# Kernel tuning notes

Measured on AMD Instinct MI355X. Metric: run time of the kernel, lower is better.

Reference implementation:

```python
import jax, jax.numpy as jnp
import numpy as np

N = 8192      # nodes
D = 256       # feature dim
E = 131072    # edges (avg degree 16)
T = 1.0       # integration horizon (single RK4 step, torchdiffeq default grid)
GAMMA = -1.0  # self-loop edge weight override


def setup_inputs() -> dict:
    key = jax.random.key(0)
    k1, k2, k3, k4 = jax.random.split(key, 4)
    h = jax.random.normal(k1, (N, D), dtype=jnp.float32)
    e = jax.random.uniform(k2, (E, 1), dtype=jnp.float32)
    src = jax.random.randint(k3, (E,), 0, N, dtype=jnp.int32)
    dst = jax.random.randint(k4, (E,), 0, N, dtype=jnp.int32)
    return {"h": h, "e": e, "src": src, "dst": dst}


def reference(h, e, src, dst):
    n = h.shape[0]
    # e[src == dst] = gamma  (self-loop override)
    e = jnp.where((src == dst)[:, None], jnp.asarray(GAMMA, e.dtype), e)

    def spmm(x):
        # DGL update_all(u_mul_e('x','e','m'), sum('m','x')):
        # out[v] = sum_{(u,v) in E} e_uv * x[u]
        return jax.ops.segment_sum(e * x[src], dst, num_segments=n)

    # ODE state is (x [N,D], K [N,N]); dx/dt = spmm(x), dK/dt = x @ x.T.
    # torchdiffeq 'rk4' = 3/8-rule fixed step; t grid [0, T] -> one step of size T.
    dt = jnp.asarray(T, h.dtype)
    x0 = h
    k1x = spmm(x0)
    xb = x0 + dt * (k1x / 3.0)
    k2x = spmm(xb)
    xc = x0 + dt * (k2x - k1x / 3.0)
    k3x = spmm(xc)
    xd = x0 + dt * (k1x - k2x + k3x)
    # K0 = 0, so final K = dt/8 * (K1 + 3*(K2 + K3) + K4), Ki = xi @ xi.T
    gram = lambda x: x @ x.T
    K = dt * 0.125 * (gram(x0) + 3.0 * (gram(xb) + gram(xc)) + gram(xd))
    return K  # [N, N], the k[:, -N:] slice returned by ODEBlock
```

## Files before the change

kernel.cpp:

```cpp
#include <hip/hip_runtime.h>
#include <hip/hip_bf16.h>
#include <stdint.h>

#define NN 8192
#define DD 256
#define EE 131072
#define KK 1024
#define BKT 32
#define NT 32
#define CAP 128

typedef __attribute__((ext_vector_type(8))) short short8;
typedef __attribute__((ext_vector_type(4))) float f32x4;

#define S1 0.35355339059327373f
#define S3 0.6123724356957945f

__device__ inline short f2bf(float x) {
  __hip_bfloat16 b = __float2bfloat16(x);
  union { __hip_bfloat16 b; short s; } u; u.b = b; return u.s;
}
__device__ inline float bf2f(short x) {
  union { unsigned u; float f; } c; c.u = ((unsigned)(unsigned short)x) << 16; return c.f;
}
__device__ inline void async_load16(const void* g, void* l) {
  __builtin_amdgcn_global_load_lds((const __attribute__((address_space(1))) void*)g,
                                   (__attribute__((address_space(3))) void*)l, 16, 0, 0);
}

__global__ void clear_k(int* __restrict__ cursor) {
  cursor[blockIdx.x * 256 + threadIdx.x] = 0;
}

__global__ void scatter_edges(const int* __restrict__ src, const int* __restrict__ dst,
                              const float* __restrict__ e, int* __restrict__ cursor,
                              int2* __restrict__ edges) {
  int i = blockIdx.x * 256 + threadIdx.x;
  if (i >= EE) return;
  int d = dst[i], s = src[i];
  int pos = atomicAdd(&cursor[d], 1);
  if (pos < CAP) {
    float w = (s == d) ? -1.0f : e[i];
    union { float f; int i; } wb; wb.f = w;
    edges[d * CAP + pos] = make_int2(s, wb.i);
  }
}

__global__ void spmm1_k(const float* __restrict__ h, const int* __restrict__ cursor,
                        const int2* __restrict__ edges, float* __restrict__ k1,
                        short* __restrict__ xbb, short* __restrict__ Y) {
  int tid = blockIdx.x * 256 + threadIdx.x;
  int v = tid >> 6, lane = tid & 63;
  int cnt = min(cursor[v], CAP);
  const int2* ev = &edges[v * CAP];
  float ax = 0.f, ay = 0.f, az = 0.f, aw = 0.f;
  for (int j = 0; j < cnt; ++j) {
    int2 ed = ev[j];
    union { int i; float f; } wb; wb.i = ed.y; float w = wb.f;
    float4 xv = *reinterpret_cast<const float4*>(&h[ed.x * DD + lane * 4]);
    ax += w * xv.x; ay += w * xv.y; az += w * xv.z; aw += w * xv.w;
  }
  int idx = v * DD + lane * 4;
  float4 hv = *reinterpret_cast<const float4*>(&h[idx]);
  float4 k; k.x = ax; k.y = ay; k.z = az; k.w = aw;
  *reinterpret_cast<float4*>(&k1[idx]) = k;
  float bx = hv.x + ax * (1.f / 3.f), by = hv.y + ay * (1.f / 3.f);
  float bz = hv.z + az * (1.f / 3.f), bw = hv.w + aw * (1.f / 3.f);
  short4 xb4; xb4.x = f2bf(bx); xb4.y = f2bf(by); xb4.z = f2bf(bz); xb4.w = f2bf(bw);
  *reinterpret_cast<short4*>(&xbb[idx]) = xb4;
  short4 y0; y0.x = f2bf(S1 * hv.x); y0.y = f2bf(S1 * hv.y);
  y0.z = f2bf(S1 * hv.z); y0.w = f2bf(S1 * hv.w);
  *reinterpret_cast<short4*>(&Y[(size_t)v * KK + lane * 4]) = y0;
  short4 yb; yb.x = f2bf(S3 * bx); yb.y = f2bf(S3 * by);
  yb.z = f2bf(S3 * bz); yb.w = f2bf(S3 * bw);
  *reinterpret_cast<short4*>(&Y[(size_t)v * KK + DD + lane * 4]) = yb;
}

__global__ void spmm2_k(const short* __restrict__ xbb, const float* __restrict__ h,
                        const float* __restrict__ k1, const int* __restrict__ cursor,
                        const int2* __restrict__ edges, short* __restrict__ xcb,
                        short* __restrict__ Y) {
  int tid = blockIdx.x * 256 + threadIdx.x;
  int v = tid >> 6, lane = tid & 63;
  int cnt = min(cursor[v], CAP);
  const int2* ev = &edges[v * CAP];
  float ax = 0.f, ay = 0.f, az = 0.f, aw = 0.f;
  for (int j = 0; j < cnt; ++j) {
    int2 ed = ev[j];
    union { int i; float f; } wb; wb.i = ed.y; float w = wb.f;
    short4 xv = *reinterpret_cast<const short4*>(&xbb[ed.x * DD + lane * 4]);
    ax += w * bf2f(xv.x); ay += w * bf2f(xv.y); az += w * bf2f(xv.z); aw += w * bf2f(xv.w);
  }
  int idx = v * DD + lane * 4;
  float4 hv = *reinterpret_cast<const float4*>(&h[idx]);
  float4 k1v = *reinterpret_cast<const float4*>(&k1[idx]);
  float cx = hv.x + ax - k1v.x * (1.f / 3.f), cy = hv.y + ay - k1v.y * (1.f / 3.f);
  float cz = hv.z + az - k1v.z * (1.f / 3.f), cw = hv.w + aw - k1v.w * (1.f / 3.f);
  short4 xc4; xc4.x = f2bf(cx); xc4.y = f2bf(cy); xc4.z = f2bf(cz); xc4.w = f2bf(cw);
  *reinterpret_cast<short4*>(&xcb[idx]) = xc4;
  short4 yc; yc.x = f2bf(S3 * cx); yc.y = f2bf(S3 * cy);
  yc.z = f2bf(S3 * cz); yc.w = f2bf(S3 * cw);
  *reinterpret_cast<short4*>(&Y[(size_t)v * KK + 2 * DD + lane * 4]) = yc;
}

__global__ void spmm3_k(const short* __restrict__ xcb, const float* __restrict__ h,
                        const float* __restrict__ k1, const int* __restrict__ cursor,
                        const int2* __restrict__ edges, short* __restrict__ Y) {
  int tid = blockIdx.x * 256 + threadIdx.x;
  int v = tid >> 6, lane = tid & 63;
  int cnt = min(cursor[v], CAP);
  const int2* ev = &edges[v * CAP];
  float ax = 0.f, ay = 0.f, az = 0.f, aw = 0.f;
  for (int j = 0; j < cnt; ++j) {
    int2 ed = ev[j];
    union { int i; float f; } wb; wb.i = ed.y; float w = wb.f;
    short4 xv = *reinterpret_cast<const short4*>(&xcb[ed.x * DD + lane * 4]);
    ax += w * bf2f(xv.x); ay += w * bf2f(xv.y); az += w * bf2f(xv.z); aw += w * bf2f(xv.w);
  }
  int idx = v * DD + lane * 4;
  float4 hv = *reinterpret_cast<const float4*>(&h[idx]);
  float4 k1v = *reinterpret_cast<const float4*>(&k1[idx]);
  short4 xc4 = *reinterpret_cast<const short4*>(&xcb[idx]);
  float dx = 2.f * hv.x + (2.f / 3.f) * k1v.x - bf2f(xc4.x) + ax;
  float dy = 2.f * hv.y + (2.f / 3.f) * k1v.y - bf2f(xc4.y) + ay;
  float dz = 2.f * hv.z + (2.f / 3.f) * k1v.z - bf2f(xc4.z) + az;
  float dw = 2.f * hv.w + (2.f / 3.f) * k1v.w - bf2f(xc4.w) + aw;
  short4 yd; yd.x = f2bf(S1 * dx); yd.y = f2bf(S1 * dy);
  yd.z = f2bf(S1 * dz); yd.w = f2bf(S1 * dw);
  *reinterpret_cast<short4*>(&Y[(size_t)v * KK + 3 * DD + lane * 4]) = yd;
}

__global__ __launch_bounds__(256, 2) void gram_gemm(const short* __restrict__ Y,
                                                    float* __restrict__ C) {
  __shared__ __attribute__((aligned(16))) short lds[36864];

  int logical = (blockIdx.x & 7) * 132 + (blockIdx.x >> 3);
  int brow = 0, rem = logical;
  while (rem >= 64 - 2 * brow) { rem -= 64 - 2 * brow; ++brow; }
  int bcol = 2 * brow + rem;

  int t = threadIdx.x;
  int lane = t & 63, wv = t >> 6;
  int wr = wv >> 1, wc = wv & 1;
  int l15 = lane & 15;
  int ksel = ((lane >> 4) ^ ((lane >> 1) & 3)) * 8;

  int srow = t >> 2;
  int scol = ((t & 3) ^ ((t >> 3) & 3)) * 8;
  const short* gA[4];
#pragma unroll
  for (int j = 0; j < 4; j++)
    gA[j] = Y + (size_t)(brow * 256 + j * 64 + srow) * KK + scol;
  const short* gB[2];
#pragma unroll
  for (int j = 0; j < 2; j++)
    gB[j] = Y + (size_t)(bcol * 128 + j * 64 + srow) * KK + scol;

  f32x4 acc[8][4] = {};

#define STAGE(tt, b) do {                                                   \
    short* base_ = lds + (b) * 12288;                                       \
    async_load16(gA[0] + (size_t)(tt) * BKT, base_ + 0 * 2048 + wv * 512);  \
    async_load16(gA[1] + (size_t)(tt) * BKT, base_ + 1 * 2048 + wv * 512);  \
    async_load16(gA[2] + (size_t)(tt) * BKT, base_ + 2 * 2048 + wv * 512);  \
    async_load16(gA[3] + (size_t)(tt) * BKT, base_ + 3 * 2048 + wv * 512);  \
    async_load16(gB[0] + (size_t)(tt) * BKT, base_ + 8192 + wv * 512);      \
    async_load16(gB[1] + (size_t)(tt) * BKT, base_ + 10240 + wv * 512);     \
  } while (0)

  STAGE(0, 0);
  STAGE(1, 1);

  for (int tt = 0; tt < NT; ++tt) {
    if (tt < NT - 1) asm volatile("s_waitcnt vmcnt(6)" ::: "memory");
    else             asm volatile("s_waitcnt vmcnt(0)" ::: "memory");
    __builtin_amdgcn_s_barrier();
    __builtin_amdgcn_sched_barrier(0);
    if (tt + 2 < NT) {
      int b = tt + 2;
      STAGE(b, b % 3);
    }

    const short* bufp = lds + (tt % 3) * 12288;
    short8 a[8], b[4];
#pragma unroll
    for (int m = 0; m < 8; m++)
      a[m] = *reinterpret_cast<const short8*>(
          &bufp[(wr * 128 + m * 16 + l15) * 32 + ksel]);
#pragma unroll
    for (int n = 0; n < 4; n++)
      b[n] = *reinterpret_cast<const short8*>(
          &bufp[8192 + (wc * 64 + n * 16 + l15) * 32 + ksel]);
    __builtin_amdgcn_s_setprio(1);
#pragma unroll
    for (int m = 0; m < 8; m++)
#pragma unroll
      for (int n = 0; n < 4; n++)
        acc[m][n] = __builtin_amdgcn_mfma_f32_16x16x32_bf16(a[m], b[n], acc[m][n], 0, 0, 0);
    __builtin_amdgcn_s_setprio(0);
  }

  int rbase = (lane >> 4) * 4;
  int row0 = brow * 256 + wr * 128;
  int colb = bcol * 128 + wc * 64;

  float* tbw = reinterpret_cast<float*>(lds) + wv * 2112;
  __builtin_amdgcn_s_barrier();
  __builtin_amdgcn_sched_barrier(0);

#pragma unroll
  for (int m = 0; m < 8; m++) {
#pragma unroll
    for (int n = 0; n < 4; n++)
#pragma unroll
      for (int r = 0; r < 4; r++)
        tbw[(rbase + r) * 68 + n * 16 + l15] = acc[m][n][r];
#pragma unroll
    for (int dr = 0; dr < 4; dr++) {
      f32x4 vv = *reinterpret_cast<const f32x4*>(
          &tbw[(dr * 4 + (lane >> 4)) * 68 + l15 * 4]);
      __builtin_nontemporal_store(
          vv, reinterpret_cast<f32x4*>(
              &C[(size_t)(row0 + m * 16 + dr * 4 + (lane >> 4)) * NN + colb + l15 * 4]));
    }
  }

#pragma unroll
  for (int n = 0; n < 4; n++) {
#pragma unroll
    for (int m = 0; m < 8; m++)
#pragma unroll
      for (int r = 0; r < 4; r++)
        tbw[l15 * 132 + m * 16 + rbase + r] = acc[m][n][r];
#pragma unroll
    for (int dr = 0; dr < 4; dr++)
#pragma unroll
      for (int half = 0; half < 2; half++) {
        f32x4 vv = *reinterpret_cast<const f32x4*>(
            &tbw[(dr * 4 + (lane >> 4)) * 132 + half * 64 + l15 * 4]);
        __builtin_nontemporal_store(
            vv, reinterpret_cast<f32x4*>(
                &C[(size_t)(colb + n * 16 + dr * 4 + (lane >> 4)) * NN +
                   row0 + half * 64 + l15 * 4]));
      }
  }
#undef STAGE
}


extern "C" void kernel_launch(void* const* d_in, const int* in_sizes, int n_in,
                              void* d_out, int out_size, void* d_ws, size_t ws_size,
                              hipStream_t stream) {
  const float* h = (const float*)d_in[0];
  const float* e = (const float*)d_in[1];
  const int* src = (const int*)d_in[2];
  const int* dst = (const int*)d_in[3];
  float* out = (float*)d_out;
  char* ws = (char*)d_ws;

  short* Y     = (short*)(ws);
  short* xbb   = (short*)(ws + 20971520);
  short* xcb   = (short*)(ws + 25165824);
  float* k1    = (float*)(ws + 29360128);
  int* cursor  = (int*)(ws + 37748736);
  int2* edges  = (int2*)(ws + 37781504);

  clear_k<<<32, 256, 0, stream>>>(cursor);
  scatter_edges<<<EE / 256, 256, 0, stream>>>(src, dst, e, cursor, edges);
  spmm1_k<<<2048, 256, 0, stream>>>(h, cursor, edges, k1, xbb, Y);
  spmm2_k<<<2048, 256, 0, stream>>>(xbb, h, k1, cursor, edges, xcb, Y);
  spmm3_k<<<2048, 256, 0, stream>>>(xcb, h, k1, cursor, edges, Y);

  gram_gemm<<<1056, 256, 0, stream>>>(Y, out);
}
```

Measured before the change: 178.6 us.

## Merge edge scatter and three SpMM stages into one cooperative kernel

Replaces the five separate launches (clear, scatter, three SpMM stages) with a single cooperative kernel that uses grid-wide syncs between phases and grid-stride loops over nodes. The goal is to remove per-launch overhead and the gaps between the small dependent kernels. In exchange, the grid is limited to 1024 blocks, each warp handles several nodes, and grid.sync barriers add their own cost.

```diff
diff --git a/kernel.cpp b/kernel.cpp
--- a/kernel.cpp
+++ b/kernel.cpp
@@ -1,6 +1,9 @@
 #include <hip/hip_runtime.h>
 #include <hip/hip_bf16.h>
+#include <hip/hip_cooperative_groups.h>
 #include <stdint.h>
+
+namespace cg = cooperative_groups;
 
 #define NN 8192
 #define DD 256
@@ -28,106 +31,105 @@
                                    (__attribute__((address_space(3))) void*)l, 16, 0, 0);
 }
 
-__global__ void clear_k(int* __restrict__ cursor) {
-  cursor[blockIdx.x * 256 + threadIdx.x] = 0;
-}
-
-__global__ void scatter_edges(const int* __restrict__ src, const int* __restrict__ dst,
-                              const float* __restrict__ e, int* __restrict__ cursor,
-                              int2* __restrict__ edges) {
-  int i = blockIdx.x * 256 + threadIdx.x;
-  if (i >= EE) return;
-  int d = dst[i], s = src[i];
-  int pos = atomicAdd(&cursor[d], 1);
-  if (pos < CAP) {
-    float w = (s == d) ? -1.0f : e[i];
-    union { float f; int i; } wb; wb.f = w;
-    edges[d * CAP + pos] = make_int2(s, wb.i);
-  }
-}
-
-__global__ void spmm1_k(const float* __restrict__ h, const int* __restrict__ cursor,
-                        const int2* __restrict__ edges, float* __restrict__ k1,
-                        short* __restrict__ xbb, short* __restrict__ Y) {
+__global__ __launch_bounds__(256, 4) void chain_k(
+    const float* __restrict__ h, const float* __restrict__ e,
+    const int* __restrict__ src, const int* __restrict__ dst,
+    int* __restrict__ cursor, int2* __restrict__ edges,
+    float* __restrict__ k1, short* __restrict__ xbb, short* __restrict__ xcb,
+    short* __restrict__ Y) {
+  cg::grid_group grid = cg::this_grid();
   int tid = blockIdx.x * 256 + threadIdx.x;
-  int v = tid >> 6, lane = tid & 63;
-  int cnt = min(cursor[v], CAP);
-  const int2* ev = &edges[v * CAP];
-  float ax = 0.f, ay = 0.f, az = 0.f, aw = 0.f;
-  for (int j = 0; j < cnt; ++j) {
-    int2 ed = ev[j];
-    union { int i; float f; } wb; wb.i = ed.y; float w = wb.f;
-    float4 xv = *reinterpret_cast<const float4*>(&h[ed.x * DD + lane * 4]);
-    ax += w * xv.x; ay += w * xv.y; az += w * xv.z; aw += w * xv.w;
-  }
-  int idx = v * DD + lane * 4;
-  float4 hv = *reinterpret_cast<const float4*>(&h[idx]);
-  float4 k; k.x = ax; k.y = ay; k.z = az; k.w = aw;
-  *reinterpret_cast<float4*>(&k1[idx]) = k;
-  float bx = hv.x + ax * (1.f / 3.f), by = hv.y + ay * (1.f / 3.f);
-  float bz = hv.z + az * (1.f / 3.f), bw = hv.w + aw * (1.f / 3.f);
-  short4 xb4; xb4.x = f2bf(bx); xb4.y = f2bf(by); xb4.z = f2bf(bz); xb4.w = f2bf(bw);
-  *reinterpret_cast<short4*>(&xbb[idx]) = xb4;
-  short4 y0; y0.x = f2bf(S1 * hv.x); y0.y = f2bf(S1 * hv.y);
-  y0.z = f2bf(S1 * hv.z); y0.w = f2bf(S1 * hv.w);
-  *reinterpret_cast<short4*>(&Y[(size_t)v * KK + lane * 4]) = y0;
-  short4 yb; yb.x = f2bf(S3 * bx); yb.y = f2bf(S3 * by);
-  yb.z = f2bf(S3 * bz); yb.w = f2bf(S3 * bw);
-  *reinterpret_cast<short4*>(&Y[(size_t)v * KK + DD + lane * 4]) = yb;
-}
-
-__global__ void spmm2_k(const short* __restrict__ xbb, const float* __restrict__ h,
-                        const float* __restrict__ k1, const int* __restrict__ cursor,
-                        const int2* __restrict__ edges, short* __restrict__ xcb,
-                        short* __restrict__ Y) {
-  int tid = blockIdx.x * 256 + threadIdx.x;
-  int v = tid >> 6, lane = tid & 63;
-  int cnt = min(cursor[v], CAP);
-  const int2* ev = &edges[v * CAP];
-  float ax = 0.f, ay = 0.f, az = 0.f, aw = 0.f;
-  for (int j = 0; j < cnt; ++j) {
-    int2 ed = ev[j];
-    union { int i; float f; } wb; wb.i = ed.y; float w = wb.f;
-    short4 xv = *reinterpret_cast<const short4*>(&xbb[ed.x * DD + lane * 4]);
-    ax += w * bf2f(xv.x); ay += w * bf2f(xv.y); az += w * bf2f(xv.z); aw += w * bf2f(xv.w);
-  }
-  int idx = v * DD + lane * 4;
-  float4 hv = *reinterpret_cast<const float4*>(&h[idx]);
-  float4 k1v = *reinterpret_cast<const float4*>(&k1[idx]);
-  float cx = hv.x + ax - k1v.x * (1.f / 3.f), cy = hv.y + ay - k1v.y * (1.f / 3.f);
-  float cz = hv.z + az - k1v.z * (1.f / 3.f), cw = hv.w + aw - k1v.w * (1.f / 3.f);
-  short4 xc4; xc4.x = f2bf(cx); xc4.y = f2bf(cy); xc4.z = f2bf(cz); xc4.w = f2bf(cw);
-  *reinterpret_cast<short4*>(&xcb[idx]) = xc4;
-  short4 yc; yc.x = f2bf(S3 * cx); yc.y = f2bf(S3 * cy);
-  yc.z = f2bf(S3 * cz); yc.w = f2bf(S3 * cw);
-  *reinterpret_cast<short4*>(&Y[(size_t)v * KK + 2 * DD + lane * 4]) = yc;
-}
-
-__global__ void spmm3_k(const short* __restrict__ xcb, const float* __restrict__ h,
-                        const float* __restrict__ k1, const int* __restrict__ cursor,
-                        const int2* __restrict__ edges, short* __restrict__ Y) {
-  int tid = blockIdx.x * 256 + threadIdx.x;
-  int v = tid >> 6, lane = tid & 63;
-  int cnt = min(cursor[v], CAP);
-  const int2* ev = &edges[v * CAP];
-  float ax = 0.f, ay = 0.f, az = 0.f, aw = 0.f;
-  for (int j = 0; j < cnt; ++j) {
-    int2 ed = ev[j];
-    union { int i; float f; } wb; wb.i = ed.y; float w = wb.f;
-    short4 xv = *reinterpret_cast<const short4*>(&xcb[ed.x * DD + lane * 4]);
-    ax += w * bf2f(xv.x); ay += w * bf2f(xv.y); az += w * bf2f(xv.z); aw += w * bf2f(xv.w);
-  }
-  int idx = v * DD + lane * 4;
-  float4 hv = *reinterpret_cast<const float4*>(&h[idx]);
-  float4 k1v = *reinterpret_cast<const float4*>(&k1[idx]);
-  short4 xc4 = *reinterpret_cast<const short4*>(&xcb[idx]);
-  float dx = 2.f * hv.x + (2.f / 3.f) * k1v.x - bf2f(xc4.x) + ax;
-  float dy = 2.f * hv.y + (2.f / 3.f) * k1v.y - bf2f(xc4.y) + ay;
-  float dz = 2.f * hv.z + (2.f / 3.f) * k1v.z - bf2f(xc4.z) + az;
-  float dw = 2.f * hv.w + (2.f / 3.f) * k1v.w - bf2f(xc4.w) + aw;
-  short4 yd; yd.x = f2bf(S1 * dx); yd.y = f2bf(S1 * dy);
-  yd.z = f2bf(S1 * dz); yd.w = f2bf(S1 * dw);
-  *reinterpret_cast<short4*>(&Y[(size_t)v * KK + 3 * DD + lane * 4]) = yd;
+  int nthreads = gridDim.x * 256;
+  int lane = tid & 63;
+  int gw = tid >> 6;
+  int nw = nthreads >> 6;
+
+  if (tid < NN) cursor[tid] = 0;
+  grid.sync();
+
+  for (int i = tid; i < EE; i += nthreads) {
+    int d = dst[i], s = src[i];
+    int pos = atomicAdd(&cursor[d], 1);
+    if (pos < CAP) {
+      float w = (s == d) ? -1.0f : e[i];
+      union { float f; int i; } wb; wb.f = w;
+      edges[d * CAP + pos] = make_int2(s, wb.i);
+    }
+  }
+  grid.sync();
+
+  for (int v = gw; v < NN; v += nw) {
+    int cnt = min(cursor[v], CAP);
+    const int2* ev = &edges[v * CAP];
+    float ax = 0.f, ay = 0.f, az = 0.f, aw = 0.f;
+    for (int j = 0; j < cnt; ++j) {
+      int2 ed = ev[j];
+      union { int i; float f; } wb; wb.i = ed.y; float w = wb.f;
+      float4 xv = *reinterpret_cast<const float4*>(&h[ed.x * DD + lane * 4]);
+      ax += w * xv.x; ay += w * xv.y; az += w * xv.z; aw += w * xv.w;
+    }
+    int idx = v * DD + lane * 4;
+    float4 hv = *reinterpret_cast<const float4*>(&h[idx]);
+    float4 k; k.x = ax; k.y = ay; k.z = az; k.w = aw;
+    *reinterpret_cast<float4*>(&k1[idx]) = k;
+    float bx = hv.x + ax * (1.f / 3.f), by = hv.y + ay * (1.f / 3.f);
+    float bz = hv.z + az * (1.f / 3.f), bw = hv.w + aw * (1.f / 3.f);
+    short4 xb4; xb4.x = f2bf(bx); xb4.y = f2bf(by); xb4.z = f2bf(bz); xb4.w = f2bf(bw);
+    *reinterpret_cast<short4*>(&xbb[idx]) = xb4;
+    short4 y0; y0.x = f2bf(S1 * hv.x); y0.y = f2bf(S1 * hv.y);
+    y0.z = f2bf(S1 * hv.z); y0.w = f2bf(S1 * hv.w);
+    *reinterpret_cast<short4*>(&Y[(size_t)v * KK + lane * 4]) = y0;
+    short4 yb; yb.x = f2bf(S3 * bx); yb.y = f2bf(S3 * by);
+    yb.z = f2bf(S3 * bz); yb.w = f2bf(S3 * bw);
+    *reinterpret_cast<short4*>(&Y[(size_t)v * KK + DD + lane * 4]) = yb;
+  }
+  grid.sync();
+
+  for (int v = gw; v < NN; v += nw) {
+    int cnt = min(cursor[v], CAP);
+    const int2* ev = &edges[v * CAP];
+    float ax = 0.f, ay = 0.f, az = 0.f, aw = 0.f;
+    for (int j = 0; j < cnt; ++j) {
+      int2 ed = ev[j];
+      union { int i; float f; } wb; wb.i = ed.y; float w = wb.f;
+      short4 xv = *reinterpret_cast<const short4*>(&xbb[ed.x * DD + lane * 4]);
+      ax += w * bf2f(xv.x); ay += w * bf2f(xv.y); az += w * bf2f(xv.z); aw += w * bf2f(xv.w);
+    }
+    int idx = v * DD + lane * 4;
+    float4 hv = *reinterpret_cast<const float4*>(&h[idx]);
+    float4 k1v = *reinterpret_cast<const float4*>(&k1[idx]);
+    float cx = hv.x + ax - k1v.x * (1.f / 3.f), cy = hv.y + ay - k1v.y * (1.f / 3.f);
+    float cz = hv.z + az - k1v.z * (1.f / 3.f), cw = hv.w + aw - k1v.w * (1.f / 3.f);
+    short4 xc4; xc4.x = f2bf(cx); xc4.y = f2bf(cy); xc4.z = f2bf(cz); xc4.w = f2bf(cw);
+    *reinterpret_cast<short4*>(&xcb[idx]) = xc4;
+    short4 yc; yc.x = f2bf(S3 * cx); yc.y = f2bf(S3 * cy);
+    yc.z = f2bf(S3 * cz); yc.w = f2bf(S3 * cw);
+    *reinterpret_cast<short4*>(&Y[(size_t)v * KK + 2 * DD + lane * 4]) = yc;
+  }
+  grid.sync();
+
+  for (int v = gw; v < NN; v += nw) {
+    int cnt = min(cursor[v], CAP);
+    const int2* ev = &edges[v * CAP];
+    float ax = 0.f, ay = 0.f, az = 0.f, aw = 0.f;
+    for (int j = 0; j < cnt; ++j) {
+      int2 ed = ev[j];
+      union { int i; float f; } wb; wb.i = ed.y; float w = wb.f;
+      short4 xv = *reinterpret_cast<const short4*>(&xcb[ed.x * DD + lane * 4]);
+      ax += w * bf2f(xv.x); ay += w * bf2f(xv.y); az += w * bf2f(xv.z); aw += w * bf2f(xv.w);
+    }
+    int idx = v * DD + lane * 4;
+    float4 hv = *reinterpret_cast<const float4*>(&h[idx]);
+    float4 k1v = *reinterpret_cast<const float4*>(&k1[idx]);
+    short4 xc4 = *reinterpret_cast<const short4*>(&xcb[idx]);
+    float dx = 2.f * hv.x + (2.f / 3.f) * k1v.x - bf2f(xc4.x) + ax;
+    float dy = 2.f * hv.y + (2.f / 3.f) * k1v.y - bf2f(xc4.y) + ay;
+    float dz = 2.f * hv.z + (2.f / 3.f) * k1v.z - bf2f(xc4.z) + az;
+    float dw = 2.f * hv.w + (2.f / 3.f) * k1v.w - bf2f(xc4.w) + aw;
+    short4 yd; yd.x = f2bf(S1 * dx); yd.y = f2bf(S1 * dy);
+    yd.z = f2bf(S1 * dz); yd.w = f2bf(S1 * dw);
+    *reinterpret_cast<short4*>(&Y[(size_t)v * KK + 3 * DD + lane * 4]) = yd;
+  }
 }
 
 __global__ __launch_bounds__(256, 2) void gram_gemm(const short* __restrict__ Y,
@@ -265,11 +267,11 @@
   int* cursor  = (int*)(ws + 37748736);
   int2* edges  = (int2*)(ws + 37781504);
 
-  clear_k<<<32, 256, 0, stream>>>(cursor);
-  scatter_edges<<<EE / 256, 256, 0, stream>>>(src, dst, e, cursor, edges);
-  spmm1_k<<<2048, 256, 0, stream>>>(h, cursor, edges, k1, xbb, Y);
-  spmm2_k<<<2048, 256, 0, stream>>>(xbb, h, k1, cursor, edges, xcb, Y);
-  spmm3_k<<<2048, 256, 0, stream>>>(xcb, h, k1, cursor, edges, Y);
+  void* args[] = {(void*)&h, (void*)&e, (void*)&src, (void*)&dst,
+                  (void*)&cursor, (void*)&edges, (void*)&k1,
+                  (void*)&xbb, (void*)&xcb, (void*)&Y};
+  hipLaunchCooperativeKernel(reinterpret_cast<void*>(chain_k),
+                             dim3(1024), dim3(256), args, 0, stream);
 
   gram_gemm<<<1056, 256, 0, stream>>>(Y, out);
 }
```

New measurement: 616.7 us. 3.45x slower.
